# Performance work log

Measured on AMD Instinct MI355X. Metric: run time of the kernel, lower is better.

## Reference

```python
import jax, jax.numpy as jnp
import numpy as np


def _assoc_scan(gates, inputs, prev=None, remove_prev=None):
    """Linear recurrence out[t] = gates[t] * out[t-1] + inputs[t], scanned over axis 1.
    gates: (B, N, 1), inputs: (B, N, D), prev: (B, D) or None."""
    if remove_prev is None:
        remove_prev = prev is not None
    if prev is not None:
        inputs = jnp.concatenate([prev[:, None, :], inputs], axis=1)
        gates = jnp.concatenate([jnp.ones_like(gates[:, :1]), gates], axis=1)

    def combine(x, y):  # x earlier, y later
        xg, xv = x
        yg, yv = y
        return (yg * xg, yg * xv + yv)

    _, out = jax.lax.associative_scan(combine, (gates, inputs), axis=1)
    if remove_prev:
        out = out[:, 1:]
    return out


def setup_inputs() -> dict:
    key = jax.random.key(0)
    ks = jax.random.split(key, 7)
    B, N, D = 32, 2048, 512  # B = batch(4) * heads(8), D = flattened per-head param dim
    O = 2                    # momentum_order
    return {
        "W_t": jax.random.normal(ks[0], (B, D), jnp.float32),
        "x_t": jax.random.normal(ks[1], (4, N, 512), jnp.float32),  # unused by forward
        "grad_l_in": jax.random.normal(ks[2], (B, N, D), jnp.float32),
        "last_momentum": jax.random.normal(ks[3], (O, B, D), jnp.float32),
        "adaptive_momentum": jax.random.uniform(ks[4], (O, B, N, 1), dtype=jnp.float32),
        "combine_momentums": jax.random.uniform(ks[5], (O + 1, B, N), dtype=jnp.float32),
        "decay_factor": jax.random.uniform(ks[6], (B, N, 1), dtype=jnp.float32),
    }


def reference(W_t, x_t, grad_l_in, last_momentum, adaptive_momentum,
              combine_momentums, decay_factor):
    surprise = grad_l_in                       # (B, N, D)
    momentum = surprise
    momentums = []
    # sequential chain over momentum orders (small fixed count)
    for o in range(adaptive_momentum.shape[0]):
        momentum = _assoc_scan(adaptive_momentum[o], momentum, prev=last_momentum[o])
        momentums.append(momentum)
    momentums = jnp.stack(momentums)           # (O, B, N, D)
    next_last_momentum = momentums[:, :, -1]   # (O, B, D)
    # learned_combine_include_zeroth: prepend raw surprise as zeroth-order momentum
    momentums = jnp.concatenate([surprise[None], momentums], axis=0)  # (O+1, B, N, D)
    update = jnp.einsum('obn,obnd->bnd', combine_momentums, momentums)
    # final decay-weighted recurrence, keeping the prepended prev (remove_prev=False)
    update = _assoc_scan(1.0 - decay_factor, update, prev=W_t, remove_prev=False)  # (B, N+1, D)
    return update, next_last_momentum
```

## Files before the change

kernel.cpp:

```cpp
#include <hip/hip_runtime.h>

#define BB 32
#define NN 2048
#define DD 512
#define CC 32
#define LL 64
#define DQ 128

typedef float vf4 __attribute__((ext_vector_type(4)));


__global__ __launch_bounds__(256) void pass1_local(
    const float* __restrict__ grad,
    const float* __restrict__ am,
    const float* __restrict__ cm,
    const float* __restrict__ dec,
    float* __restrict__ Mtot,
    float* __restrict__ local_end)
{
    const int half = __builtin_amdgcn_readfirstlane(threadIdx.x >> 7);
    const int lane = threadIdx.x & 127;
    const int c = (blockIdx.x << 1) | half;
    const int b = blockIdx.y;
    const vf4* g4 = (const vf4*)grad;

    const float* a0p = am + (size_t)(0 * BB + b) * NN;
    const float* a1p = am + (size_t)(1 * BB + b) * NN;
    const float* c0p = cm + (size_t)(0 * BB + b) * NN;
    const float* c1p = cm + (size_t)(1 * BB + b) * NN;
    const float* c2p = cm + (size_t)(2 * BB + b) * NN;
    const float* dp  = dec + (size_t)b * NN;

    vf4 m0 = {0.f, 0.f, 0.f, 0.f}, m1 = m0, w = m0;
    float p00 = 1.f, p10 = 0.f, p11 = 1.f, p20 = 0.f, p21 = 0.f, p22 = 1.f;

    const int t0 = c * LL;
    #pragma unroll 8
    for (int t = t0; t < t0 + LL; ++t) {
        const float a0 = a0p[t], a1 = a1p[t];
        const float c0 = c0p[t], c1 = c1p[t], c2 = c2p[t];
        const float e  = 1.0f - dp[t];
        const vf4 g = g4[(size_t)(b * NN + t) * DQ + lane];

        m0 = a0 * m0 + g;
        m1 = a1 * m1 + m0;
        w  = e * w + c0 * g + c1 * m0 + c2 * m1;

        const float k0 = (c1 + c2) * a0;
        const float k1 = c2 * a1;
        const float n00 = a0 * p00;
        const float n10 = fmaf(a0, p00, a1 * p10);
        const float n11 = a1 * p11;
        const float n20 = fmaf(k0, p00, fmaf(k1, p10, e * p20));
        const float n21 = fmaf(k1, p11, e * p21);
        const float n22 = e * p22;
        p00 = n00; p10 = n10; p11 = n11; p20 = n20; p21 = n21; p22 = n22;
    }

    vf4* le = (vf4*)local_end;
    const size_t base = (size_t)(b * CC + c) * 3 * DQ;
    le[base + 0 * DQ + lane] = m0;
    le[base + 1 * DQ + lane] = m1;
    le[base + 2 * DQ + lane] = w;

    if (lane == 0) {
        float* mt = Mtot + (size_t)(b * CC + c) * 6;
        mt[0] = p00; mt[1] = p10; mt[2] = p11;
        mt[3] = p20; mt[4] = p21; mt[5] = p22;
    }
}

__global__ __launch_bounds__(256) void pass3_fused(
    const float* __restrict__ grad,
    const float* __restrict__ am,
    const float* __restrict__ cm,
    const float* __restrict__ dec,
    const float* __restrict__ Wt,
    const float* __restrict__ lm,
    const float* __restrict__ Mtot,
    const float* __restrict__ local_end,
    float* __restrict__ out)
{
    const int half = __builtin_amdgcn_readfirstlane(threadIdx.x >> 7);
    const int lane = threadIdx.x & 127;
    const int c = (blockIdx.x << 1) | half;
    const int b = blockIdx.y;

    vf4 s0 = ((const vf4*)lm)[(size_t)(0 * BB + b) * DQ + lane];
    vf4 s1 = ((const vf4*)lm)[(size_t)(1 * BB + b) * DQ + lane];
    vf4 s2 = ((const vf4*)Wt)[(size_t)b * DQ + lane];

    const vf4* le = (const vf4*)local_end;
    for (int cc = 0; cc < c; ++cc) {
        const float* mt = Mtot + (size_t)(b * CC + cc) * 6;
        const float p00 = mt[0], p10 = mt[1], p11 = mt[2];
        const float p20 = mt[3], p21 = mt[4], p22 = mt[5];

        const size_t base = (size_t)(b * CC + cc) * 3 * DQ;
        const vf4 l0 = le[base + 0 * DQ + lane];
        const vf4 l1 = le[base + 1 * DQ + lane];
        const vf4 l2 = le[base + 2 * DQ + lane];

        const vf4 n0 = p00 * s0 + l0;
        const vf4 n1 = p10 * s0 + p11 * s1 + l1;
        const vf4 n2 = p20 * s0 + p21 * s1 + p22 * s2 + l2;
        s0 = n0; s1 = n1; s2 = n2;
    }

    vf4* out4 = (vf4*)out;
    if (c == 0) {
        __builtin_nontemporal_store(s2, &out4[(size_t)(b * (NN + 1)) * DQ + lane]);
    }

    const float* a0p = am + (size_t)(0 * BB + b) * NN;
    const float* a1p = am + (size_t)(1 * BB + b) * NN;
    const float* c0p = cm + (size_t)(0 * BB + b) * NN;
    const float* c1p = cm + (size_t)(1 * BB + b) * NN;
    const float* c2p = cm + (size_t)(2 * BB + b) * NN;
    const float* dp  = dec + (size_t)b * NN;

    const vf4* g4 = (const vf4*)grad;
    vf4 m0 = s0, m1 = s1, w = s2;

    const int t0 = c * LL;
    #pragma unroll 8
    for (int t = t0; t < t0 + LL; ++t) {
        const float a0 = a0p[t], a1 = a1p[t];
        const float c0 = c0p[t], c1 = c1p[t], c2 = c2p[t];
        const float e  = 1.0f - dp[t];
        const vf4 g = g4[(size_t)(b * NN + t) * DQ + lane];

        m0 = a0 * m0 + g;
        m1 = a1 * m1 + m0;
        w  = e * w + c0 * g + c1 * m0 + c2 * m1;

        __builtin_nontemporal_store(
            w, &out4[(size_t)(b * (NN + 1) + t + 1) * DQ + lane]);
    }

    if (c == CC - 1) {
        const size_t nl = (size_t)BB * (NN + 1) * DQ;
        __builtin_nontemporal_store(m0, &out4[nl + (size_t)(0 * BB + b) * DQ + lane]);
        __builtin_nontemporal_store(m1, &out4[nl + (size_t)(1 * BB + b) * DQ + lane]);
    }
}

extern "C" void kernel_launch(void* const* d_in, const int* in_sizes, int n_in,
                              void* d_out, int out_size, void* d_ws, size_t ws_size,
                              hipStream_t stream) {
    const float* Wt   = (const float*)d_in[0];
    const float* grad = (const float*)d_in[2];
    const float* lm   = (const float*)d_in[3];
    const float* am   = (const float*)d_in[4];
    const float* cm   = (const float*)d_in[5];
    const float* dec  = (const float*)d_in[6];
    float* out = (float*)d_out;

    char* ws = (char*)d_ws;
    float* Mtot      = (float*)ws;
    float* local_end = (float*)(ws + (size_t)BB * CC * 6 * sizeof(float));

    dim3 grid(CC / 2, BB);
    pass1_local<<<grid, 256, 0, stream>>>(grad, am, cm, dec, Mtot, local_end);
    pass3_fused<<<grid, 256, 0, stream>>>(grad, am, cm, dec, Wt, lm, Mtot,
                                          local_end, out);
}
```

Before: 74.50 us.

## Split carry propagation into a dedicated sequential kernel between passes

Replaces the per-chunk redundant prefix recomputation of chunk carries with a separate kernel that scans chunk summaries once per batch and writes per-chunk starting states to workspace. The streaming pass then loads its carry directly instead of looping over all earlier chunks. This removes quadratic redundant reads of local_end and Mtot, at the cost of an extra kernel launch and a serial, low-parallelism carry kernel with only one block per batch.

```diff
diff --git a/kernel.cpp b/kernel.cpp
--- a/kernel.cpp
+++ b/kernel.cpp
@@ -70,33 +70,38 @@
     }
 }
 
-__global__ __launch_bounds__(256) void pass3_fused(
-    const float* __restrict__ grad,
-    const float* __restrict__ am,
-    const float* __restrict__ cm,
-    const float* __restrict__ dec,
+__global__ __launch_bounds__(128) void pass2_carry(
     const float* __restrict__ Wt,
     const float* __restrict__ lm,
     const float* __restrict__ Mtot,
     const float* __restrict__ local_end,
+    float* __restrict__ carry,
     float* __restrict__ out)
 {
-    const int half = __builtin_amdgcn_readfirstlane(threadIdx.x >> 7);
-    const int lane = threadIdx.x & 127;
-    const int c = (blockIdx.x << 1) | half;
-    const int b = blockIdx.y;
+    const int b = blockIdx.x;
+    const int lane = threadIdx.x;
 
     vf4 s0 = ((const vf4*)lm)[(size_t)(0 * BB + b) * DQ + lane];
     vf4 s1 = ((const vf4*)lm)[(size_t)(1 * BB + b) * DQ + lane];
     vf4 s2 = ((const vf4*)Wt)[(size_t)b * DQ + lane];
 
+    vf4* out4 = (vf4*)out;
+    __builtin_nontemporal_store(s2, &out4[(size_t)(b * (NN + 1)) * DQ + lane]);
+
+    vf4* cy = (vf4*)carry;
     const vf4* le = (const vf4*)local_end;
-    for (int cc = 0; cc < c; ++cc) {
-        const float* mt = Mtot + (size_t)(b * CC + cc) * 6;
+
+    #pragma unroll 8
+    for (int c = 0; c < CC; ++c) {
+        const size_t base = (size_t)(b * CC + c) * 3 * DQ;
+        cy[base + 0 * DQ + lane] = s0;
+        cy[base + 1 * DQ + lane] = s1;
+        cy[base + 2 * DQ + lane] = s2;
+
+        const float* mt = Mtot + (size_t)(b * CC + c) * 6;
         const float p00 = mt[0], p10 = mt[1], p11 = mt[2];
         const float p20 = mt[3], p21 = mt[4], p22 = mt[5];
 
-        const size_t base = (size_t)(b * CC + cc) * 3 * DQ;
         const vf4 l0 = le[base + 0 * DQ + lane];
         const vf4 l1 = le[base + 1 * DQ + lane];
         const vf4 l2 = le[base + 2 * DQ + lane];
@@ -107,10 +112,29 @@
         s0 = n0; s1 = n1; s2 = n2;
     }
 
-    vf4* out4 = (vf4*)out;
-    if (c == 0) {
-        __builtin_nontemporal_store(s2, &out4[(size_t)(b * (NN + 1)) * DQ + lane]);
-    }
+    const size_t nl = (size_t)BB * (NN + 1) * DQ;
+    __builtin_nontemporal_store(s0, &out4[nl + (size_t)(0 * BB + b) * DQ + lane]);
+    __builtin_nontemporal_store(s1, &out4[nl + (size_t)(1 * BB + b) * DQ + lane]);
+}
+
+__global__ __launch_bounds__(256) void pass3_stream(
+    const float* __restrict__ grad,
+    const float* __restrict__ am,
+    const float* __restrict__ cm,
+    const float* __restrict__ dec,
+    const float* __restrict__ carry,
+    float* __restrict__ out)
+{
+    const int half = __builtin_amdgcn_readfirstlane(threadIdx.x >> 7);
+    const int lane = threadIdx.x & 127;
+    const int c = (blockIdx.x << 1) | half;
+    const int b = blockIdx.y;
+
+    const vf4* cy = (const vf4*)carry;
+    const size_t cb = (size_t)(b * CC + c) * 3 * DQ;
+    vf4 m0 = cy[cb + 0 * DQ + lane];
+    vf4 m1 = cy[cb + 1 * DQ + lane];
+    vf4 w  = cy[cb + 2 * DQ + lane];
 
     const float* a0p = am + (size_t)(0 * BB + b) * NN;
     const float* a1p = am + (size_t)(1 * BB + b) * NN;
@@ -120,7 +144,7 @@
     const float* dp  = dec + (size_t)b * NN;
 
     const vf4* g4 = (const vf4*)grad;
-    vf4 m0 = s0, m1 = s1, w = s2;
+    vf4* out4 = (vf4*)out;
 
     const int t0 = c * LL;
     #pragma unroll 8
@@ -136,12 +160,6 @@
 
         __builtin_nontemporal_store(
             w, &out4[(size_t)(b * (NN + 1) + t + 1) * DQ + lane]);
-    }
-
-    if (c == CC - 1) {
-        const size_t nl = (size_t)BB * (NN + 1) * DQ;
-        __builtin_nontemporal_store(m0, &out4[nl + (size_t)(0 * BB + b) * DQ + lane]);
-        __builtin_nontemporal_store(m1, &out4[nl + (size_t)(1 * BB + b) * DQ + lane]);
     }
 }
 
@@ -159,9 +177,10 @@
     char* ws = (char*)d_ws;
     float* Mtot      = (float*)ws;
     float* local_end = (float*)(ws + (size_t)BB * CC * 6 * sizeof(float));
+    float* carry     = local_end + (size_t)BB * CC * 3 * DD;
 
     dim3 grid(CC / 2, BB);
     pass1_local<<<grid, 256, 0, stream>>>(grad, am, cm, dec, Mtot, local_end);
-    pass3_fused<<<grid, 256, 0, stream>>>(grad, am, cm, dec, Wt, lm, Mtot,
-                                          local_end, out);
+    pass2_carry<<<BB, 128, 0, stream>>>(Wt, lm, Mtot, local_end, carry, out);
+    pass3_stream<<<grid, 256, 0, stream>>>(grad, am, cm, dec, carry, out);
 }
```

Measured after the change: 80.99 us. 8.7% more time.
